# Performance work log

Hardware: AMD Instinct MI355X
Metric: run time of the kernel (lower is better)

Reference implementation:

```python
import jax, jax.numpy as jnp
import numpy as np

GRID_SIZE = 5
SPLINE_ORDER = 3
GRID_RANGE = (-6.0, 6.0)


def make_grid(in_features):
    h = (GRID_RANGE[1] - GRID_RANGE[0]) / GRID_SIZE
    g = np.arange(-SPLINE_ORDER, GRID_SIZE + SPLINE_ORDER + 1, dtype=np.float32) * h + GRID_RANGE[0]
    return jnp.asarray(np.tile(g[None, :], (in_features, 1)))  # (in, grid_size + 2*order + 1)


def b_splines(x, grid):
    # x: (b, in)  grid: (in, G)  -> bases: (b, in, grid_size + spline_order)
    xg = x[:, :, None]
    bases = ((xg >= grid[:, :-1]) & (xg < grid[:, 1:])).astype(x.dtype)
    for k in range(1, SPLINE_ORDER + 1):
        left = (xg - grid[:, : -(k + 1)]) / (grid[:, k:-1] - grid[:, : -(k + 1)]) * bases[:, :, :-1]
        right = (grid[:, k + 1:] - xg) / (grid[:, k + 1:] - grid[:, 1:-k]) * bases[:, :, 1:]
        bases = left + right
    return bases


def kan_linear(x, grid, base_w, spline_w, scaler):
    # base path: SiLU activation then linear
    base_out = jax.nn.silu(x) @ base_w.T
    # spline path: B-spline basis then per-(out,in,basis) weighted sum
    bases = b_splines(x, grid)                      # (b, in, K)
    sw = spline_w * scaler[:, :, None]              # standalone spline scaler
    spline_out = jnp.einsum('bik,oik->bo', bases, sw)
    return base_out + spline_out


def setup_inputs() -> dict:
    key = jax.random.key(0)
    ks = jax.random.split(key, 7)
    b, c, H, W = 32, 512, 64, 64
    hidden = max(16, c // 8)
    x = jax.random.normal(ks[0], (b, c, H, W), dtype=jnp.float32)
    scale = 0.1
    return {
        'x': x,
        'grid1': make_grid(c),
        'base_w1': jax.random.normal(ks[1], (hidden, c), dtype=jnp.float32) * scale,
        'spline_w1': jax.random.normal(ks[2], (hidden, c, GRID_SIZE + SPLINE_ORDER), dtype=jnp.float32) * scale,
        'scaler1': jax.random.normal(ks[3], (hidden, c), dtype=jnp.float32) * scale + 1.0,
        'grid2': make_grid(hidden),
        'base_w2': jax.random.normal(ks[4], (c, hidden), dtype=jnp.float32) * scale,
        'spline_w2': jax.random.normal(ks[5], (c, hidden, GRID_SIZE + SPLINE_ORDER), dtype=jnp.float32) * scale,
        'scaler2': jax.random.normal(ks[6], (c, hidden), dtype=jnp.float32) * scale + 1.0,
    }


def reference(x, grid1, base_w1, spline_w1, scaler1, grid2, base_w2, spline_w2, scaler2):
    b, c = x.shape[0], x.shape[1]
    s = jnp.mean(x, axis=(2, 3))                    # adaptive_avg_pool2d to 1x1
    s = jnp.nan_to_num(s)
    s = kan_linear(s, grid1, base_w1, spline_w1, scaler1)
    s = jax.nn.silu(s)
    s = kan_linear(s, grid2, base_w2, spline_w2, scaler2)
    gate = jax.nn.sigmoid(s).reshape(b, c, 1, 1)
    return x * gate
```

## Files before the change

### kernel.cpp

```cpp
#include <hip/hip_runtime.h>
#include <math.h>

#define B 32
#define C 512
#define HIDDEN 64
#define HW 4096
#define NBASES 8
#define NKNOTS 12

__device__ __forceinline__ float wave_reduce(float v) {
    #pragma unroll
    for (int m = 32; m > 0; m >>= 1) v += __shfl_xor(v, m, 64);
    return v;
}

__device__ __forceinline__ float silu_f(float x) {
    return x / (1.0f + __expf(-x));
}

__device__ __forceinline__ void compute_bases(float x, const float* g, float* out) {
    float b[11];
    #pragma unroll
    for (int j = 0; j < 11; ++j)
        b[j] = (x >= g[j] && x < g[j + 1]) ? 1.0f : 0.0f;
    #pragma unroll
    for (int k = 1; k <= 3; ++k) {
        #pragma unroll
        for (int j = 0; j + k < 11; ++j) {
            float left  = (x - g[j]) / (g[j + k] - g[j]) * b[j];
            float right = (g[j + k + 1] - x) / (g[j + k + 1] - g[j + 1]) * b[j + 1];
            b[j] = left + right;
        }
    }
    #pragma unroll
    for (int j = 0; j < NBASES; ++j) out[j] = b[j];
}

__global__ __launch_bounds__(256) void mean_kernel(const float* __restrict__ x,
                                                   float* __restrict__ s) {
    const int plane = blockIdx.x;
    const float4* xp = (const float4*)(x + (size_t)plane * HW);
    float acc = 0.0f;
    #pragma unroll
    for (int j = 0; j < 4; ++j) {
        float4 v = xp[threadIdx.x + j * 256];
        acc += (v.x + v.y) + (v.z + v.w);
    }
    acc = wave_reduce(acc);
    __shared__ float partial[4];
    const int wave = threadIdx.x >> 6, lane = threadIdx.x & 63;
    if (lane == 0) partial[wave] = acc;
    __syncthreads();
    if (threadIdx.x == 0) {
        float m = ((partial[0] + partial[1]) + (partial[2] + partial[3])) * (1.0f / (float)HW);
        if (isnan(m)) m = 0.0f;
        if (isinf(m)) m = (m > 0.f) ? 3.4028235e38f : -3.4028235e38f;
        s[plane] = m;
    }
}

__global__ __launch_bounds__(256) void kan_kernel(
        const float* __restrict__ s,
        const float* __restrict__ grid1,
        const float* __restrict__ bw1,
        const float* __restrict__ sw1,
        const float* __restrict__ sc1,
        const float* __restrict__ grid2,
        const float* __restrict__ bw2,
        const float* __restrict__ sw2,
        const float* __restrict__ sc2,
        float* __restrict__ gate)
{
    const int b = blockIdx.x;
    const int tid = threadIdx.x;
    const int wave = tid >> 6, lane = tid & 63;

    __shared__ float feat1[C * 9];
    __shared__ float s1raw[HIDDEN];
    __shared__ float feat2[HIDDEN * 9];

    float g1[NKNOTS], g2[NKNOTS];
    #pragma unroll
    for (int j = 0; j < NKNOTS; ++j) { g1[j] = grid1[j]; g2[j] = grid2[j]; }

    #pragma unroll
    for (int r = 0; r < 2; ++r) {
        const int f = tid + r * 256;
        const float xv = s[b * C + f];
        float* dst = &feat1[f * 9];
        dst[0] = silu_f(xv);
        compute_bases(xv, g1, dst + 1);
    }
    __syncthreads();

    for (int o = wave; o < HIDDEN; o += 4) {
        const float* bw = bw1 + o * C;
        const float* sw = sw1 + o * C * NBASES;
        const float* sc = sc1 + o * C;
        float acc = 0.0f;
        #pragma unroll
        for (int ii = 0; ii < C / 64; ++ii) {
            const int i = ii * 64 + lane;
            const float* f = &feat1[i * 9];
            float t = 0.0f;
            #pragma unroll
            for (int k = 0; k < NBASES; ++k) t += f[1 + k] * sw[i * NBASES + k];
            acc += f[0] * bw[i] + t * sc[i];
        }
        acc = wave_reduce(acc);
        if (lane == 0) s1raw[o] = acc;
    }
    __syncthreads();

    if (tid < HIDDEN) {
        const float x2 = silu_f(s1raw[tid]);
        float* dst = &feat2[tid * 9];
        dst[0] = silu_f(x2);
        compute_bases(x2, g2, dst + 1);
    }
    __syncthreads();

    for (int o = wave; o < C; o += 4) {
        const int i = lane;
        const float* f = &feat2[i * 9];
        float t = 0.0f;
        #pragma unroll
        for (int k = 0; k < NBASES; ++k) t += f[1 + k] * sw2[(o * HIDDEN + i) * NBASES + k];
        float acc = f[0] * bw2[o * HIDDEN + i] + t * sc2[o * HIDDEN + i];
        acc = wave_reduce(acc);
        if (lane == 0) gate[b * C + o] = 1.0f / (1.0f + __expf(-acc));
    }
}

__global__ __launch_bounds__(256) void scale_kernel(const float4* __restrict__ x,
                                                    const float* __restrict__ gate,
                                                    float4* __restrict__ out) {
    const int idx = blockIdx.x * 256 + threadIdx.x;
    const int plane = idx >> 10;
    const float g = gate[plane];
    float4 v = x[idx];
    v.x *= g; v.y *= g; v.z *= g; v.w *= g;
    out[idx] = v;
}

extern "C" void kernel_launch(void* const* d_in, const int* in_sizes, int n_in,
                              void* d_out, int out_size, void* d_ws, size_t ws_size,
                              hipStream_t stream) {
    const float* x     = (const float*)d_in[0];
    const float* grid1 = (const float*)d_in[1];
    const float* bw1   = (const float*)d_in[2];
    const float* sw1   = (const float*)d_in[3];
    const float* sc1   = (const float*)d_in[4];
    const float* grid2 = (const float*)d_in[5];
    const float* bw2   = (const float*)d_in[6];
    const float* sw2   = (const float*)d_in[7];
    const float* sc2   = (const float*)d_in[8];
    float* out  = (float*)d_out;

    float* s    = (float*)d_ws;
    float* gate = s + B * C;

    mean_kernel<<<B * C, 256, 0, stream>>>(x, s);
    kan_kernel<<<B, 256, 0, stream>>>(s, grid1, bw1, sw1, sc1,
                                      grid2, bw2, sw2, sc2, gate);
    scale_kernel<<<(B * C * HW / 4) / 256, 256, 0, stream>>>(
        (const float4*)x, gate, (float4*)out);
}
```

Baseline: 659.4 us.

## Split KAN stage into parallel per-output kernels and restructure mean/scale kernels

Replaces the single 32-block KAN kernel with two kernels. The first spreads hidden outputs across 512 blocks and applies SiLU. The second computes one output channel per wave across 4096 blocks, recomputing the bases per wave. The mean kernel now reduces one plane per wave without shared memory, and the scale kernel handles one plane per block with a single gate load. This is meant to remove the serial latency of the under-parallelised KAN stage, at the cost of an extra launch and redundant basis computation.

```diff
diff --git a/kernel.cpp b/kernel.cpp
--- a/kernel.cpp
+++ b/kernel.cpp
@@ -38,109 +38,113 @@
 
 __global__ __launch_bounds__(256) void mean_kernel(const float* __restrict__ x,
                                                    float* __restrict__ s) {
-    const int plane = blockIdx.x;
+    const int wave = threadIdx.x >> 6, lane = threadIdx.x & 63;
+    const int plane = blockIdx.x * 4 + wave;
     const float4* xp = (const float4*)(x + (size_t)plane * HW);
     float acc = 0.0f;
     #pragma unroll
-    for (int j = 0; j < 4; ++j) {
-        float4 v = xp[threadIdx.x + j * 256];
+    for (int j = 0; j < 16; ++j) {
+        float4 v = xp[lane + j * 64];
         acc += (v.x + v.y) + (v.z + v.w);
     }
     acc = wave_reduce(acc);
-    __shared__ float partial[4];
-    const int wave = threadIdx.x >> 6, lane = threadIdx.x & 63;
-    if (lane == 0) partial[wave] = acc;
-    __syncthreads();
-    if (threadIdx.x == 0) {
-        float m = ((partial[0] + partial[1]) + (partial[2] + partial[3])) * (1.0f / (float)HW);
+    if (lane == 0) {
+        float m = acc * (1.0f / (float)HW);
         if (isnan(m)) m = 0.0f;
         if (isinf(m)) m = (m > 0.f) ? 3.4028235e38f : -3.4028235e38f;
         s[plane] = m;
     }
 }
 
-__global__ __launch_bounds__(256) void kan_kernel(
+__global__ __launch_bounds__(256) void kan1_kernel(
         const float* __restrict__ s,
         const float* __restrict__ grid1,
         const float* __restrict__ bw1,
         const float* __restrict__ sw1,
         const float* __restrict__ sc1,
+        float* __restrict__ s1x2)
+{
+    const int b     = blockIdx.x >> 4;
+    const int obase = (blockIdx.x & 15) << 2;
+    const int tid = threadIdx.x;
+    const int wave = tid >> 6, lane = tid & 63;
+
+    __shared__ float feat[C * 9];
+
+    float g1[NKNOTS];
+    #pragma unroll
+    for (int j = 0; j < NKNOTS; ++j) g1[j] = grid1[j];
+
+    #pragma unroll
+    for (int r = 0; r < 2; ++r) {
+        const int f = tid + r * 256;
+        const float xv = s[b * C + f];
+        float* dst = &feat[f * 9];
+        dst[0] = silu_f(xv);
+        compute_bases(xv, g1, dst + 1);
+    }
+    __syncthreads();
+
+    const int o = obase + wave;
+    const float* bw = bw1 + o * C;
+    const float* sw = sw1 + (size_t)o * C * NBASES;
+    const float* sc = sc1 + o * C;
+    float acc = 0.0f;
+    #pragma unroll
+    for (int ii = 0; ii < C / 64; ++ii) {
+        const int i = ii * 64 + lane;
+        const float* f = &feat[i * 9];
+        float t = 0.0f;
+        #pragma unroll
+        for (int k = 0; k < NBASES; ++k) t += f[1 + k] * sw[i * NBASES + k];
+        acc += f[0] * bw[i] + t * sc[i];
+    }
+    acc = wave_reduce(acc);
+    if (lane == 0) s1x2[b * HIDDEN + o] = silu_f(acc);
+}
+
+__global__ __launch_bounds__(256) void kan2_kernel(
+        const float* __restrict__ s1x2,
         const float* __restrict__ grid2,
         const float* __restrict__ bw2,
         const float* __restrict__ sw2,
         const float* __restrict__ sc2,
         float* __restrict__ gate)
 {
-    const int b = blockIdx.x;
-    const int tid = threadIdx.x;
-    const int wave = tid >> 6, lane = tid & 63;
+    const int wave = threadIdx.x >> 6, lane = threadIdx.x & 63;
+    const int gw = blockIdx.x * 4 + wave;
+    const int b = gw >> 9, o = gw & 511;
 
-    __shared__ float feat1[C * 9];
-    __shared__ float s1raw[HIDDEN];
-    __shared__ float feat2[HIDDEN * 9];
+    float g2[NKNOTS];
+    #pragma unroll
+    for (int j = 0; j < NKNOTS; ++j) g2[j] = grid2[j];
 
-    float g1[NKNOTS], g2[NKNOTS];
+    const float x2 = s1x2[b * HIDDEN + lane];
+    float bs[NBASES];
+    compute_bases(x2, g2, bs);
+
+    const int wi = o * HIDDEN + lane;
+    float t = 0.0f;
     #pragma unroll
-    for (int j = 0; j < NKNOTS; ++j) { g1[j] = grid1[j]; g2[j] = grid2[j]; }
+    for (int k = 0; k < NBASES; ++k) t += bs[k] * sw2[(size_t)wi * NBASES + k];
+    float acc = silu_f(x2) * bw2[wi] + t * sc2[wi];
 
-    #pragma unroll
-    for (int r = 0; r < 2; ++r) {
-        const int f = tid + r * 256;
-        const float xv = s[b * C + f];
-        float* dst = &feat1[f * 9];
-        dst[0] = silu_f(xv);
-        compute_bases(xv, g1, dst + 1);
-    }
-    __syncthreads();
-
-    for (int o = wave; o < HIDDEN; o += 4) {
-        const float* bw = bw1 + o * C;
-        const float* sw = sw1 + o * C * NBASES;
-        const float* sc = sc1 + o * C;
-        float acc = 0.0f;
-        #pragma unroll
-        for (int ii = 0; ii < C / 64; ++ii) {
-            const int i = ii * 64 + lane;
-            const float* f = &feat1[i * 9];
-            float t = 0.0f;
-            #pragma unroll
-            for (int k = 0; k < NBASES; ++k) t += f[1 + k] * sw[i * NBASES + k];
-            acc += f[0] * bw[i] + t * sc[i];
-        }
-        acc = wave_reduce(acc);
-        if (lane == 0) s1raw[o] = acc;
-    }
-    __syncthreads();
-
-    if (tid < HIDDEN) {
-        const float x2 = silu_f(s1raw[tid]);
-        float* dst = &feat2[tid * 9];
-        dst[0] = silu_f(x2);
-        compute_bases(x2, g2, dst + 1);
-    }
-    __syncthreads();
-
-    for (int o = wave; o < C; o += 4) {
-        const int i = lane;
-        const float* f = &feat2[i * 9];
-        float t = 0.0f;
-        #pragma unroll
-        for (int k = 0; k < NBASES; ++k) t += f[1 + k] * sw2[(o * HIDDEN + i) * NBASES + k];
-        float acc = f[0] * bw2[o * HIDDEN + i] + t * sc2[o * HIDDEN + i];
-        acc = wave_reduce(acc);
-        if (lane == 0) gate[b * C + o] = 1.0f / (1.0f + __expf(-acc));
-    }
+    acc = wave_reduce(acc);
+    if (lane == 0) gate[b * C + o] = 1.0f / (1.0f + __expf(-acc));
 }
 
 __global__ __launch_bounds__(256) void scale_kernel(const float4* __restrict__ x,
                                                     const float* __restrict__ gate,
                                                     float4* __restrict__ out) {
-    const int idx = blockIdx.x * 256 + threadIdx.x;
-    const int plane = idx >> 10;
-    const float g = gate[plane];
-    float4 v = x[idx];
-    v.x *= g; v.y *= g; v.z *= g; v.w *= g;
-    out[idx] = v;
+    const float g = gate[blockIdx.x];
+    const float4* xp = x + (size_t)blockIdx.x * (HW / 4);
+    float4* op = out + (size_t)blockIdx.x * (HW / 4);
+    #pragma unroll
+    for (int j = 0; j < 4; ++j) {
+        float4 v = xp[threadIdx.x + j * 256];
+        v.x *= g; v.y *= g; v.z *= g; v.w *= g;
+        op[threadIdx.x + j * 256] = v;
+    }
 }
 
 extern "C" void kernel_launch(void* const* d_in, const int* in_sizes, int n_in,
@@ -158,11 +162,11 @@
     float* out  = (float*)d_out;
 
     float* s    = (float*)d_ws;
-    float* gate = s + B * C;
+    float* s1x2 = s + B * C;
+    float* gate = s1x2 + B * HIDDEN;
 
-    mean_kernel<<<B * C, 256, 0, stream>>>(x, s);
-    kan_kernel<<<B, 256, 0, stream>>>(s, grid1, bw1, sw1, sc1,
-                                      grid2, bw2, sw2, sc2, gate);
-    scale_kernel<<<(B * C * HW / 4) / 256, 256, 0, stream>>>(
-        (const float4*)x, gate, (float4*)out);
+    mean_kernel<<<B * C / 4, 256, 0, stream>>>(x, s);
+    kan1_kernel<<<B * (HIDDEN / 4), 256, 0, stream>>>(s, grid1, bw1, sw1, sc1, s1x2);
+    kan2_kernel<<<B * C / 4, 256, 0, stream>>>(s1x2, grid2, bw2, sw2, sc2, gate);
+    scale_kernel<<<B * C, 256, 0, stream>>>((const float4*)x, gate, (float4*)out);
 }
```

Result: faster. 528.5 us (-19.9%).
